# Kernel optimization log

Measured on AMD Instinct MI355X. Metric: run time of the kernel, lower is better.

Reference implementation:

```python
import jax, jax.numpy as jnp
import numpy as np

EMBED_DIM = 1024
NUM_HEADS = 16
HEAD_DIM = EMBED_DIM // NUM_HEADS
WINDOW = 256


def setup_inputs() -> dict:
    key = jax.random.key(0)
    ks = jax.random.split(key, 9)
    B, S, E = 4, 4096, EMBED_DIM
    sc = 1.0 / np.sqrt(E)
    return {
        "x": jax.random.normal(ks[0], (B, S, E), jnp.float32),
        "Wq": jax.random.normal(ks[1], (E, E), jnp.float32) * sc,
        "bq": jax.random.normal(ks[2], (E,), jnp.float32) * 0.01,
        "Wk": jax.random.normal(ks[3], (E, E), jnp.float32) * sc,
        "bk": jax.random.normal(ks[4], (E,), jnp.float32) * 0.01,
        "Wv": jax.random.normal(ks[5], (E, E), jnp.float32) * sc,
        "bv": jax.random.normal(ks[6], (E,), jnp.float32) * 0.01,
        "Wo": jax.random.normal(ks[7], (E, E), jnp.float32) * sc,
        "bo": jax.random.normal(ks[8], (E,), jnp.float32) * 0.01,
    }


def reference(x, Wq, bq, Wk, bk, Wv, bv, Wo, bo):
    B, S, E = x.shape
    H, D, W = NUM_HEADS, HEAD_DIM, WINDOW
    NW = S // W  # seq_len chosen divisible by window -> no padding

    def split_heads(t):  # [B,S,E] -> [B,H,NW,W,D]
        return t.reshape(B, S, H, D).transpose(0, 2, 1, 3).reshape(B, H, NW, W, D)

    q = split_heads(x @ Wq + bq)
    k = split_heads(x @ Wk + bk)
    v = split_heads(x @ Wv + bv)

    # block-diagonal attention within each non-overlapping window
    scores = jnp.einsum("bhnqd,bhnkd->bhnqk", q, k) / jnp.sqrt(
        jnp.asarray(D, x.dtype))
    attn = jax.nn.softmax(scores, axis=-1)
    out = jnp.einsum("bhnqk,bhnkd->bhnqd", attn, v)  # [B,H,NW,W,D]

    out = out.reshape(B, H, S, D).transpose(0, 2, 1, 3).reshape(B, S, E)
    return out @ Wo + bo
```

## Files before the change

### kernel.cpp

```cpp
#include <hip/hip_runtime.h>

typedef __bf16 bf16x8 __attribute__((ext_vector_type(8)));
typedef float  f32x4  __attribute__((ext_vector_type(4)));

#define MFMA(a,b,c) __builtin_amdgcn_mfma_f32_16x16x32_bf16((a),(b),(c),0,0,0)
#define VMC(N) asm volatile("s_waitcnt vmcnt(" #N ")" ::: "memory")

__device__ __forceinline__ unsigned short f2bf(float f){
  unsigned u = __builtin_bit_cast(unsigned, f);
  u += 0x7fffu + ((u>>16)&1u);
  return (unsigned short)(u>>16);
}
__device__ __forceinline__ unsigned pack_bf2(float a, float b){
  return (unsigned)f2bf(a) | ((unsigned)f2bf(b)<<16);
}
__device__ __forceinline__ void gload_lds16(const void* g, void* l){
  __builtin_amdgcn_global_load_lds((__attribute__((address_space(1))) void*)(g),
                                   (__attribute__((address_space(3))) void*)(l), 16, 0, 0);
}

__global__ void k_cvt(const float* __restrict__ x,
                      const float* __restrict__ Wq, const float* __restrict__ Wk,
                      const float* __restrict__ Wv, const float* __restrict__ Wo,
                      unsigned short* __restrict__ xbf, unsigned short* __restrict__ wT){
  __shared__ float tile[32][33];
  const int bb = blockIdx.x;
  if (bb < 4096){
    const size_t t = (size_t)bb*256 + threadIdx.x;
    #pragma unroll
    for (int i=0;i<4;i++){
      size_t idx = t + (size_t)i*1048576;
      float4 f = ((const float4*)x)[idx];
      ((uint2*)xbf)[idx] = make_uint2(pack_bf2(f.x,f.y), pack_bf2(f.z,f.w));
    }
  } else {
    const int zz = bb - 4096;
    const int z = zz>>10;
    const float* W = (z==0)?Wq:(z==1)?Wk:(z==2)?Wv:Wo;
    unsigned short* out = wT + (size_t)z*1048576;
    const int r0 = ((zz>>5)&31)*32, c0 = (zz&31)*32;
    const int r = threadIdx.x>>5, c = threadIdx.x&31;
    #pragma unroll
    for (int i=0;i<4;i++) tile[r + i*8][c] = W[(size_t)(r0 + r + i*8)*1024 + c0 + c];
    __syncthreads();
    #pragma unroll
    for (int i=0;i<4;i++)
      out[(size_t)(c0 + r + i*8)*1024 + r0 + c] = f2bf(tile[c][r + i*8]);
  }
}

#define QUAD16(AF, BF, MF0) do { \
  _Pragma("unroll") \
  for (int mf_=0; mf_<4; ++mf_){ \
    _Pragma("unroll") \
    for (int nf_=0; nf_<4; ++nf_) \
      acc[MF0+mf_][nf_] = MFMA(AF[mf_], BF[nf_], acc[MF0+mf_][nf_]); \
  } } while(0)

#define RDA(DST, MF0, P) do { \
  _Pragma("unroll") \
  for (int mf_=0; mf_<4; ++mf_) \
    DST[mf_] = *(const bf16x8*)((P) + ((MF0)+mf_)*2048); \
  } while(0)

#define RDB(DST, P) do { \
  _Pragma("unroll") \
  for (int nf_=0; nf_<4; ++nf_) \
    DST[nf_] = *(const bf16x8*)((P) + nf_*2048); \
  } while(0)

#define STG2(P0, P1, DT, ISA, BUF, HF) do { \
  char* _ld = smem + ((ISA)?0:65536) + (BUF)*32768 + (HF)*16384 + wid*1024; \
  gload_lds16((P0) + (DT), _ld); \
  gload_lds16((P1) + (DT), _ld + 8192); \
  } while(0)

#define PH_OPEN   __builtin_amdgcn_s_barrier(); __builtin_amdgcn_s_setprio(1)
#define PH_CLOSE  __builtin_amdgcn_s_setprio(0)
#define PH_END    __builtin_amdgcn_s_barrier()

#define TB(u) ((((u)>>4)*2097152) + (((u)&15)<<7))
#define TA(u) (((u)&15)<<7)

template<int MODE>
__global__ __launch_bounds__(512,2) void k_gemm8(const unsigned short* __restrict__ A,
                       const unsigned short* __restrict__ Bm,
                       const float* __restrict__ bias0, const float* __restrict__ bias1,
                       const float* __restrict__ bias2,
                       unsigned short* __restrict__ q_ws, unsigned short* __restrict__ k_ws,
                       unsigned short* __restrict__ v_ws, float* __restrict__ outf)
{
  __shared__ char smem[131072];
  const int tid = threadIdx.x, lane = tid&63, wid = tid>>6;
  const int g = lane>>4, l15 = lane&15;
  const int wr = wid>>2, wc = wid&3;

  constexpr int NZ = (MODE==0)? 3 : 1;
  const int x  = blockIdx.x & 7;
  const int c  = blockIdx.x >> 3;
  const int m0 = ((c>>2)*8 + x) << 8;
  const int nE = (c&3) << 8;

  f32x4 acc[8][4];
  #pragma unroll
  for (int i=0;i<8;i++)
    #pragma unroll
    for (int j=0;j<4;j++) acc[i][j] = f32x4{0.f,0.f,0.f,0.f};

  const int sw = (l15&7)<<4;
  const int brow = (wc&1)*64;

  const char* dsA00 = smem + wr*16384 + l15*128 + ((g*16) ^ sw);
  const char* dsA01 = smem + wr*16384 + l15*128 + ((64+g*16) ^ sw);
  const char* dsA10 = dsA00 + 32768;
  const char* dsA11 = dsA01 + 32768;
  const char* dsB00 = smem + 65536 + (wc>>1)*16384 + (brow+l15)*128 + ((g*16) ^ sw);
  const char* dsB01 = smem + 65536 + (wc>>1)*16384 + (brow+l15)*128 + ((64+g*16) ^ sw);
  const char* dsB10 = dsB00 + 32768;
  const char* dsB11 = dsB01 + 32768;

  const int rj = tid>>3;
  const int cs = ((tid*16)&127) ^ ((rj&7)<<4);
  const char* pgA0_0 = (const char*)A  + (size_t)(m0 +       rj)*2048 + cs;
  const char* pgA0_1 = (const char*)A  + (size_t)(m0 +  64 + rj)*2048 + cs;
  const char* pgA1_0 = (const char*)A  + (size_t)(m0 + 128 + rj)*2048 + cs;
  const char* pgA1_1 = (const char*)A  + (size_t)(m0 + 192 + rj)*2048 + cs;
  const char* pgB0_0 = (const char*)Bm + (size_t)(nE +       rj)*2048 + cs;
  const char* pgB0_1 = (const char*)Bm + (size_t)(nE +  64 + rj)*2048 + cs;
  const char* pgB1_0 = (const char*)Bm + (size_t)(nE + 128 + rj)*2048 + cs;
  const char* pgB1_1 = (const char*)Bm + (size_t)(nE + 192 + rj)*2048 + cs;

  bf16x8 aF[4], bF[4];

  auto epi = [&](int z){
    if constexpr (MODE==0){
      const float* bias = (z==0)? bias0 : (z==1)? bias1 : bias2;
      if (z==2){
        #pragma unroll
        for (int nf=0;nf<4;nf++){
          const int ncol = nE + wc*64 + nf*16 + l15;
          const float bn = bias[ncol];
          const int h = ncol>>6, d = ncol&63;
          #pragma unroll
          for (int mf=0;mf<8;mf++){
            const int mb = m0 + wr*128 + mf*16 + g*4;
            const int b = mb>>12, s = mb&4095, nw = s>>8, w0 = s&255;
            unsigned short pk0=f2bf(acc[mf][nf][0]+bn), pk1=f2bf(acc[mf][nf][1]+bn),
                           pk2=f2bf(acc[mf][nf][2]+bn), pk3=f2bf(acc[mf][nf][3]+bn);
            size_t idx = ((((size_t)(b*16+h)*16 + nw)*64 + d)<<8) + w0;
            *(ushort4*)(v_ws + idx) = make_ushort4(pk0,pk1,pk2,pk3);
          }
        }
      } else {
        unsigned short* dst = (z==0)? q_ws : k_ws;
        const float scale = (z==0)? 0.125f : 1.0f;
        #pragma unroll
        for (int nf=0;nf<4;nf++){
          const int ncol = nE + wc*64 + nf*16 + l15;
          const float bn = bias[ncol];
          const int h = ncol>>6, d = ncol&63;
          #pragma unroll
          for (int mf=0;mf<8;mf++){
            const int mb = m0 + wr*128 + mf*16 + g*4;
            #pragma unroll
            for (int r=0;r<4;r++){
              const int m = mb + r, b = m>>12, s = m&4095;
              dst[(((size_t)(b*16+h)*4096 + s)<<6) + d] = f2bf((acc[mf][nf][r]+bn)*scale);
            }
          }
        }
      }
      #pragma unroll
      for (int i=0;i<8;i++)
        #pragma unroll
        for (int j=0;j<4;j++) acc[i][j] = f32x4{0.f,0.f,0.f,0.f};
    }
  };

  STG2(pgA0_0, pgA0_1, TA(0), 1, 0, 0);
  STG2(pgA1_0, pgA1_1, TA(0), 1, 0, 1);
  STG2(pgB0_0, pgB0_1, TB(0), 0, 0, 0);
  STG2(pgB1_0, pgB1_1, TB(0), 0, 0, 1);
  STG2(pgB0_0, pgB0_1, TB(1), 0, 1, 0);
  VMC(2);
  __builtin_amdgcn_s_barrier();

  #pragma unroll 1
  for (int j=0;j<8*NZ-1;++j){
    const int T = 2*j;
    RDA(aF,0,dsA00); RDB(bF,dsB00); STG2(pgB1_0,pgB1_1,TB(T+1),0,1,1);
    PH_OPEN; QUAD16(aF,bF,0); PH_CLOSE; PH_END;
    RDA(aF,4,dsA00); STG2(pgA0_0,pgA0_1,TA(T+1),1,1,0);
    PH_OPEN; QUAD16(aF,bF,4); PH_CLOSE; PH_END;
    RDA(aF,0,dsA01); RDB(bF,dsB01); STG2(pgA1_0,pgA1_1,TA(T+1),1,1,1);
    PH_OPEN; QUAD16(aF,bF,0); PH_CLOSE; PH_END;
    RDA(aF,4,dsA01); STG2(pgB0_0,pgB0_1,TB(T+2),0,0,0);
    PH_OPEN; QUAD16(aF,bF,4); PH_CLOSE; VMC(2); PH_END;
    RDA(aF,0,dsA10); RDB(bF,dsB10); STG2(pgB1_0,pgB1_1,TB(T+2),0,0,1);
    PH_OPEN; QUAD16(aF,bF,0); PH_CLOSE; PH_END;
    RDA(aF,4,dsA10); STG2(pgA0_0,pgA0_1,TA(T+2),1,0,0);
    PH_OPEN; QUAD16(aF,bF,4); PH_CLOSE; PH_END;
    RDA(aF,0,dsA11); RDB(bF,dsB11); STG2(pgA1_0,pgA1_1,TA(T+2),1,0,1);
    PH_OPEN; QUAD16(aF,bF,0); PH_CLOSE; PH_END;
    RDA(aF,4,dsA11); STG2(pgB0_0,pgB0_1,TB(T+3),0,1,0);
    PH_OPEN; QUAD16(aF,bF,4); PH_CLOSE; VMC(2); PH_END;
    if (MODE==0 && (j&7)==7) epi(j>>3);
  }
  {
    RDA(aF,0,dsA00); RDB(bF,dsB00); STG2(pgB1_0,pgB1_1,TB(16*NZ-1),0,1,1);
    PH_OPEN; QUAD16(aF,bF,0); PH_CLOSE; PH_END;
    RDA(aF,4,dsA00); STG2(pgA0_0,pgA0_1,TA(16*NZ-1),1,1,0);
    PH_OPEN; QUAD16(aF,bF,4); PH_CLOSE; PH_END;
    RDA(aF,0,dsA01); RDB(bF,dsB01); STG2(pgA1_0,pgA1_1,TA(16*NZ-1),1,1,1);
    PH_OPEN; QUAD16(aF,bF,0); PH_CLOSE; PH_END;
    RDA(aF,4,dsA01);
    PH_OPEN; QUAD16(aF,bF,4); PH_CLOSE; VMC(0); PH_END;
    RDA(aF,0,dsA10); RDB(bF,dsB10);
    PH_OPEN; QUAD16(aF,bF,0); PH_CLOSE; PH_END;
    RDA(aF,4,dsA10);
    PH_OPEN; QUAD16(aF,bF,4); PH_CLOSE; PH_END;
    RDA(aF,0,dsA11); RDB(bF,dsB11);
    PH_OPEN; QUAD16(aF,bF,0); PH_CLOSE; PH_END;
    RDA(aF,4,dsA11);
    PH_OPEN; QUAD16(aF,bF,4); PH_CLOSE; PH_END;
  }

  if constexpr (MODE==0){
    epi(2);
  } else {
    #pragma unroll
    for (int nf=0;nf<4;nf++){
      const int n = nE + wc*64 + nf*16 + l15;
      const float bn = bias0[n];
      #pragma unroll
      for (int mf=0;mf<8;mf++)
        #pragma unroll
        for (int r=0;r<4;r++){
          const int m = m0 + wr*128 + mf*16 + g*4 + r;
          outf[(size_t)m*1024 + n] = acc[mf][nf][r] + bn;
        }
    }
  }
}

__global__ __launch_bounds__(256,2) void k_attn(const unsigned short* __restrict__ qw,
                                                const unsigned short* __restrict__ kw,
                                                const unsigned short* __restrict__ vw,
                                                unsigned short* __restrict__ ow)
{
  __shared__ unsigned short Ks[2][4096];
  __shared__ unsigned short Vs[2][4096];
  __shared__ unsigned short Ps[4][4096];
  const int tid = threadIdx.x, lane = tid&63, wid = tid>>6;
  const int g = lane>>4, l15 = lane&15;
  const int bhn = blockIdx.x;
  const int nw = bhn&15, h = (bhn>>4)&15, b = bhn>>8;

  const size_t qkbase = ((size_t)((b*16+h)*4096 + nw*256))<<6;
  const unsigned short* Qg = qw + qkbase;
  const unsigned short* Kg = kw + qkbase;
  const unsigned short* Vg = vw + (((size_t)(b*16+h)*16 + nw)<<14);
  const float NEG_INF = -__builtin_inff();

  bf16x8 qa[4][2];
  #pragma unroll
  for (int qf=0;qf<4;qf++)
    #pragma unroll
    for (int ks=0;ks<2;ks++)
      qa[qf][ks] = *(const bf16x8*)((const char*)Qg + (wid*64 + qf*16 + l15)*128 + ks*64 + g*16);

  auto stage = [&](int kt, int bi){
    #pragma unroll
    for (int i=0;i<4;i++){
      const int chunk = wid*4 + i;
      const int obase = (chunk&7)<<10;
      const int o = obase + lane*16;
      const int r = o>>7, cb = o&127;
      const int cs = cb ^ ((r&7)<<4);
      if (chunk < 8)
        gload_lds16((const char*)Kg + (kt*64 + r)*128 + cs, (char*)Ks[bi] + obase);
      else
        gload_lds16((const char*)Vg + r*512 + kt*128 + cs, (char*)Vs[bi] + obase);
    }
  };

  f32x4 oacc[4][4];
  float mrow[4][4], lrow[4][4];
  #pragma unroll
  for (int i=0;i<4;i++)
    #pragma unroll
    for (int j=0;j<4;j++){ oacc[i][j] = f32x4{0.f,0.f,0.f,0.f}; mrow[i][j] = NEG_INF; lrow[i][j] = 0.f; }

  stage(0,0);
  __syncthreads();
  for (int kt=0;kt<4;kt++){
    const int cur = kt&1;
    if (kt<3) stage(kt+1, cur^1);

    bf16x8 kb[4][2];
    #pragma unroll
    for (int kf=0;kf<4;kf++)
      #pragma unroll
      for (int ks=0;ks<2;ks++){
        const int kr = kf*16 + l15, cb = ks*64 + g*16;
        kb[kf][ks] = *(const bf16x8*)((const char*)Ks[cur] + kr*128 + (cb ^ ((kr&7)<<4)));
      }

    unsigned short* P = Ps[wid];
    #pragma unroll
    for (int qf=0;qf<4;qf++){
      f32x4 sfr[4];
      #pragma unroll
      for (int kf=0;kf<4;kf++){
        f32x4 zz = f32x4{0.f,0.f,0.f,0.f};
        zz = MFMA(qa[qf][0], kb[kf][0], zz);
        sfr[kf] = MFMA(qa[qf][1], kb[kf][1], zz);
      }
      #pragma unroll
      for (int r=0;r<4;r++){
        float t = fmaxf(fmaxf(sfr[0][r],sfr[1][r]), fmaxf(sfr[2][r],sfr[3][r]));
        t = fmaxf(t, __shfl_xor(t,1,64)); t = fmaxf(t, __shfl_xor(t,2,64));
        t = fmaxf(t, __shfl_xor(t,4,64)); t = fmaxf(t, __shfl_xor(t,8,64));
        const float mo = mrow[qf][r];
        const float mn = fmaxf(mo, t);
        const float alpha = __expf(mo - mn);
        float rs = 0.f;
        #pragma unroll
        for (int kf=0;kf<4;kf++){ float p = __expf(sfr[kf][r]-mn); sfr[kf][r] = p; rs += p; }
        rs += __shfl_xor(rs,1,64); rs += __shfl_xor(rs,2,64);
        rs += __shfl_xor(rs,4,64); rs += __shfl_xor(rs,8,64);
        lrow[qf][r] = lrow[qf][r]*alpha + rs;
        mrow[qf][r] = mn;
        #pragma unroll
        for (int df=0;df<4;df++) oacc[qf][df][r] *= alpha;
        const int prow = qf*16 + g*4 + r;
        const int sw = (prow&7)<<4;
        char* Pb = (char*)P + prow*128;
        #pragma unroll
        for (int kf=0;kf<4;kf++)
          *(unsigned short*)(Pb + (((kf*16 + l15)*2) ^ sw)) = f2bf(sfr[kf][r]);
      }
    }
    __builtin_amdgcn_sched_barrier(0);

    bf16x8 vb[4][2];
    #pragma unroll
    for (int df=0;df<4;df++)
      #pragma unroll
      for (int ks=0;ks<2;ks++){
        const int d = df*16 + l15, cb = ks*64 + g*16;
        vb[df][ks] = *(const bf16x8*)((const char*)Vs[cur] + d*128 + (cb ^ ((d&7)<<4)));
      }
    #pragma unroll
    for (int qf=0;qf<4;qf++){
      const int pr = qf*16 + l15;
      const bf16x8 pa0 = *(const bf16x8*)((const char*)P + pr*128 + ((g*16)      ^ ((pr&7)<<4)));
      const bf16x8 pa1 = *(const bf16x8*)((const char*)P + pr*128 + ((64 + g*16) ^ ((pr&7)<<4)));
      #pragma unroll
      for (int df=0;df<4;df++){
        oacc[qf][df] = MFMA(pa0, vb[df][0], oacc[qf][df]);
        oacc[qf][df] = MFMA(pa1, vb[df][1], oacc[qf][df]);
      }
    }
    __syncthreads();
  }

  #pragma unroll
  for (int qf=0;qf<4;qf++)
    #pragma unroll
    for (int r=0;r<4;r++){
      const float inv = 1.f / lrow[qf][r];
      const int srow = nw*256 + wid*64 + qf*16 + g*4 + r;
      const size_t base = ((size_t)b*4096 + srow)*1024 + (size_t)h*64;
      #pragma unroll
      for (int df=0;df<4;df++)
        ow[base + df*16 + l15] = f2bf(oacc[qf][df][r]*inv);
    }
}

extern "C" void kernel_launch(void* const* d_in, const int* in_sizes, int n_in,
                              void* d_out, int out_size, void* d_ws, size_t ws_size,
                              hipStream_t stream)
{
  const float* x  = (const float*)d_in[0];
  const float* Wq = (const float*)d_in[1];
  const float* bq = (const float*)d_in[2];
  const float* Wk = (const float*)d_in[3];
  const float* bk = (const float*)d_in[4];
  const float* Wv = (const float*)d_in[5];
  const float* bv = (const float*)d_in[6];
  const float* Wo = (const float*)d_in[7];
  const float* bo = (const float*)d_in[8];
  float* out = (float*)d_out;

  char* ws = (char*)d_ws;
  unsigned short* xbf  = (unsigned short*)(ws);
  unsigned short* wT   = (unsigned short*)(ws + (size_t)32*1048576);
  unsigned short* q_ws = (unsigned short*)(ws + (size_t)40*1048576);
  unsigned short* k_ws = (unsigned short*)(ws + (size_t)72*1048576);
  unsigned short* v_ws = (unsigned short*)(ws + (size_t)104*1048576);
  unsigned short* obf  = xbf;

  k_cvt<<<8192,256,0,stream>>>(x, Wq,Wk,Wv,Wo, xbf, wT);
  k_gemm8<0><<<256,512,0,stream>>>(xbf, wT, bq,bk,bv, q_ws,k_ws,v_ws, nullptr);
  k_attn<<<1024,256,0,stream>>>(q_ws,k_ws,v_ws, obf);
  k_gemm8<1><<<256,512,0,stream>>>(obf, wT + (size_t)3*1048576, bo,nullptr,nullptr,
                                   nullptr,nullptr,nullptr, out);
}
```

Before: 263.2 us.

## Double-buffer LDS fragment registers to overlap reads with MFMA phases

The GEMM main loop now keeps two register sets for A and B fragments and issues the LDS reads for the next phase inside the current MFMA phase, instead of reading and then computing serially. The per-phase closing barrier is dropped, leaving one barrier per phase plus a mid-tile barrier after the global-load wait. The goal is to hide LDS read latency behind matrix instructions and cut barrier count. In exchange it roughly doubles the fragment registers, which could hurt occupancy at launch bounds (512,2), and it changes when buffers may be overwritten, which risks races.

```diff
diff --git a/kernel.cpp b/kernel.cpp
--- a/kernel.cpp
+++ b/kernel.cpp
@@ -75,9 +75,9 @@
   gload_lds16((P1) + (DT), _ld + 8192); \
   } while(0)
 
-#define PH_OPEN   __builtin_amdgcn_s_barrier(); __builtin_amdgcn_s_setprio(1)
-#define PH_CLOSE  __builtin_amdgcn_s_setprio(0)
-#define PH_END    __builtin_amdgcn_s_barrier()
+#define PH   __builtin_amdgcn_s_barrier(); __builtin_amdgcn_s_setprio(1)
+#define PHX  __builtin_amdgcn_s_setprio(0)
+#define MIDBAR __builtin_amdgcn_s_barrier()
 
 #define TB(u) ((((u)>>4)*2097152) + (((u)&15)<<7))
 #define TA(u) (((u)&15)<<7)
@@ -96,6 +96,7 @@
   const int wr = wid>>2, wc = wid&3;
 
   constexpr int NZ = (MODE==0)? 3 : 1;
+  constexpr int NT = 16*NZ;
   const int x  = blockIdx.x & 7;
   const int c  = blockIdx.x >> 3;
   const int m0 = ((c>>2)*8 + x) << 8;
@@ -130,7 +131,7 @@
   const char* pgB1_0 = (const char*)Bm + (size_t)(nE + 128 + rj)*2048 + cs;
   const char* pgB1_1 = (const char*)Bm + (size_t)(nE + 192 + rj)*2048 + cs;
 
-  bf16x8 aF[4], bF[4];
+  bf16x8 aA[4], bA[4], aB[4], bB[4];
 
   auto epi = [&](int z){
     if constexpr (MODE==0){
@@ -184,45 +185,32 @@
   STG2(pgB0_0, pgB0_1, TB(1), 0, 1, 0);
   VMC(2);
   __builtin_amdgcn_s_barrier();
+  RDA(aA,0,dsA00); RDB(bA,dsB00);
 
   #pragma unroll 1
   for (int j=0;j<8*NZ-1;++j){
     const int T = 2*j;
-    RDA(aF,0,dsA00); RDB(bF,dsB00); STG2(pgB1_0,pgB1_1,TB(T+1),0,1,1);
-    PH_OPEN; QUAD16(aF,bF,0); PH_CLOSE; PH_END;
-    RDA(aF,4,dsA00); STG2(pgA0_0,pgA0_1,TA(T+1),1,1,0);
-    PH_OPEN; QUAD16(aF,bF,4); PH_CLOSE; PH_END;
-    RDA(aF,0,dsA01); RDB(bF,dsB01); STG2(pgA1_0,pgA1_1,TA(T+1),1,1,1);
-    PH_OPEN; QUAD16(aF,bF,0); PH_CLOSE; PH_END;
-    RDA(aF,4,dsA01); STG2(pgB0_0,pgB0_1,TB(T+2),0,0,0);
-    PH_OPEN; QUAD16(aF,bF,4); PH_CLOSE; VMC(2); PH_END;
-    RDA(aF,0,dsA10); RDB(bF,dsB10); STG2(pgB1_0,pgB1_1,TB(T+2),0,0,1);
-    PH_OPEN; QUAD16(aF,bF,0); PH_CLOSE; PH_END;
-    RDA(aF,4,dsA10); STG2(pgA0_0,pgA0_1,TA(T+2),1,0,0);
-    PH_OPEN; QUAD16(aF,bF,4); PH_CLOSE; PH_END;
-    RDA(aF,0,dsA11); RDB(bF,dsB11); STG2(pgA1_0,pgA1_1,TA(T+2),1,0,1);
-    PH_OPEN; QUAD16(aF,bF,0); PH_CLOSE; PH_END;
-    RDA(aF,4,dsA11); STG2(pgB0_0,pgB0_1,TB(T+3),0,1,0);
-    PH_OPEN; QUAD16(aF,bF,4); PH_CLOSE; VMC(2); PH_END;
+    PH; QUAD16(aA,bA,0); RDA(aB,4,dsA00); STG2(pgB1_0,pgB1_1,TB(T+1),0,1,1); PHX;
+    PH; QUAD16(aB,bA,4); RDA(aA,0,dsA01); RDB(bB,dsB01); STG2(pgA0_0,pgA0_1,TA(T+1),1,1,0); PHX;
+    PH; QUAD16(aA,bB,0); RDA(aB,4,dsA01); STG2(pgA1_0,pgA1_1,TA(T+1),1,1,1); PHX;
+    PH; QUAD16(aB,bB,4); STG2(pgB0_0,pgB0_1,TB(T+2),0,0,0); VMC(2); MIDBAR;
+        RDA(aA,0,dsA10); RDB(bA,dsB10); PHX;
+    PH; QUAD16(aA,bA,0); RDA(aB,4,dsA10); STG2(pgB1_0,pgB1_1,TB(T+2),0,0,1); PHX;
+    PH; QUAD16(aB,bA,4); RDA(aA,0,dsA11); RDB(bB,dsB11); STG2(pgA0_0,pgA0_1,TA(T+2),1,0,0); PHX;
+    PH; QUAD16(aA,bB,0); RDA(aB,4,dsA11); STG2(pgA1_0,pgA1_1,TA(T+2),1,0,1); PHX;
+    PH; QUAD16(aB,bB,4); STG2(pgB0_0,pgB0_1,TB(T+3),0,1,0); VMC(2); MIDBAR;
+        RDA(aA,0,dsA00); RDB(bA,dsB00); PHX;
     if (MODE==0 && (j&7)==7) epi(j>>3);
   }
   {
-    RDA(aF,0,dsA00); RDB(bF,dsB00); STG2(pgB1_0,pgB1_1,TB(16*NZ-1),0,1,1);
-    PH_OPEN; QUAD16(aF,bF,0); PH_CLOSE; PH_END;
-    RDA(aF,4,dsA00); STG2(pgA0_0,pgA0_1,TA(16*NZ-1),1,1,0);
-    PH_OPEN; QUAD16(aF,bF,4); PH_CLOSE; PH_END;
-    RDA(aF,0,dsA01); RDB(bF,dsB01); STG2(pgA1_0,pgA1_1,TA(16*NZ-1),1,1,1);
-    PH_OPEN; QUAD16(aF,bF,0); PH_CLOSE; PH_END;
-    RDA(aF,4,dsA01);
-    PH_OPEN; QUAD16(aF,bF,4); PH_CLOSE; VMC(0); PH_END;
-    RDA(aF,0,dsA10); RDB(bF,dsB10);
-    PH_OPEN; QUAD16(aF,bF,0); PH_CLOSE; PH_END;
-    RDA(aF,4,dsA10);
-    PH_OPEN; QUAD16(aF,bF,4); PH_CLOSE; PH_END;
-    RDA(aF,0,dsA11); RDB(bF,dsB11);
-    PH_OPEN; QUAD16(aF,bF,0); PH_CLOSE; PH_END;
-    RDA(aF,4,dsA11);
-    PH_OPEN; QUAD16(aF,bF,4); PH_CLOSE; PH_END;
+    PH; QUAD16(aA,bA,0); RDA(aB,4,dsA00); STG2(pgB1_0,pgB1_1,TB(NT-1),0,1,1); PHX;
+    PH; QUAD16(aB,bA,4); RDA(aA,0,dsA01); RDB(bB,dsB01); STG2(pgA0_0,pgA0_1,TA(NT-1),1,1,0); PHX;
+    PH; QUAD16(aA,bB,0); RDA(aB,4,dsA01); STG2(pgA1_0,pgA1_1,TA(NT-1),1,1,1); PHX;
+    PH; QUAD16(aB,bB,4); VMC(0); MIDBAR; RDA(aA,0,dsA10); RDB(bA,dsB10); PHX;
+    PH; QUAD16(aA,bA,0); RDA(aB,4,dsA10); PHX;
+    PH; QUAD16(aB,bA,4); RDA(aA,0,dsA11); RDB(bB,dsB11); PHX;
+    PH; QUAD16(aA,bB,0); RDA(aB,4,dsA11); PHX;
+    PH; QUAD16(aB,bB,4); PHX;
   }
 
   if constexpr (MODE==0){
```

After: 260.7 us (median of 2 runs). No clear change (-1.0%).
